# Performance work log

Hardware: AMD Instinct MI355X
Metric: run time of the kernel (lower is better)

## Reference

```python
import jax, jax.numpy as jnp
import numpy as np

EMBED_DIM = 768
N_HEADS = 12
SEQ_LEN = 577
MAX_REL = 2


def _relative_position_indices(seq_len: int, max_rel: int) -> jnp.ndarray:
    """Static [S, S] int index map into the relative bias table."""
    n_patches = seq_len - 1
    n_per_dim = int(np.sqrt(n_patches))
    n_entries = (2 * max_rel - 1) ** 2
    cls_cls, cls_patch, patch_cls = n_entries, n_entries + 1, n_entries + 2
    idx = np.arange(seq_len)
    qy, qx = (idx - 1) // n_per_dim, (idx - 1) % n_per_dim
    ry = np.clip(qy[:, None] - qy[None, :], -max_rel + 1, max_rel - 1)
    rx = np.clip(qx[:, None] - qx[None, :], -max_rel + 1, max_rel - 1)
    patch_idx = (ry + max_rel - 1) * (2 * max_rel - 1) + (rx + max_rel - 1)
    is_cls = idx == 0
    out = np.where(is_cls[None, :], patch_cls, patch_idx)
    out = np.where(is_cls[:, None], cls_patch, out)
    out = np.where(is_cls[:, None] & is_cls[None, :], cls_cls, out)
    return jnp.asarray(out, dtype=jnp.int32)


def setup_inputs() -> dict:
    key = jax.random.key(0)
    ks = jax.random.split(key, 6)
    e = EMBED_DIM
    scale = 1.0 / np.sqrt(e)
    return {
        "x": jax.random.normal(ks[0], (32, SEQ_LEN, e), dtype=jnp.float32),
        "Wq": jax.random.normal(ks[1], (e, e), dtype=jnp.float32) * scale,
        "Wk": jax.random.normal(ks[2], (e, e), dtype=jnp.float32) * scale,
        "Wv": jax.random.normal(ks[3], (e, e), dtype=jnp.float32) * scale,
        "Wo": jax.random.normal(ks[4], (e, e), dtype=jnp.float32) * scale,
        "bo": jnp.zeros((e,), dtype=jnp.float32),
        "bias_table": jax.random.normal(ks[5], (12,), dtype=jnp.float32) * 0.02,
    }


def reference(x, Wq, Wk, Wv, Wo, bo, bias_table):
    b, s, e = x.shape
    h, d = N_HEADS, e // N_HEADS
    rel_idx = _relative_position_indices(s, MAX_REL)  # [S, S] int32 (static)

    q = (x @ Wq).reshape(b, s, h, d).transpose(0, 2, 1, 3)  # [b,h,s,d]
    k = (x @ Wk).reshape(b, s, h, d).transpose(0, 2, 1, 3)
    v = (x @ Wv).reshape(b, s, h, d).transpose(0, 2, 1, 3)

    scores = jnp.einsum('bhqd,bhkd->bhqk', q, k) / jnp.sqrt(jnp.float32(d))
    bias = jnp.take(bias_table, rel_idx, axis=0)  # [S, S]
    attn = jax.nn.softmax(scores + bias[None, None, :, :], axis=-1)

    out = jnp.einsum('bhqk,bhkd->bhqd', attn, v)
    out = out.transpose(0, 2, 1, 3).reshape(b, s, e)
    return out @ Wo + bo
```

## Files before the change

kernel.cpp:

```cpp
#include <hip/hip_runtime.h>

typedef unsigned short u16;
typedef short short8 __attribute__((ext_vector_type(8)));
typedef float floatx4 __attribute__((ext_vector_type(4)));

#define MFMA16(a, b, c) __builtin_amdgcn_mfma_f32_16x16x32_bf16((a), (b), (c), 0, 0, 0)

__device__ __forceinline__ u16 f2bf(float f) {
  unsigned u = __builtin_bit_cast(unsigned, f);
  u = (u + 0x7fffu + ((u >> 16) & 1u)) >> 16;
  return (u16)u;
}

__device__ __forceinline__ float bf2f(u16 u) {
  return __builtin_bit_cast(float, ((unsigned)u) << 16);
}

__device__ __forceinline__ float exp2hw(float x) {
  float r; asm("v_exp_f32 %0, %1" : "=v"(r) : "v"(x)); return r;
}

__device__ __forceinline__ unsigned cvtpk_bf16(float lo, float hi) {
  unsigned r;
  asm("v_cvt_pk_bf16_f32 %0, %1, %2" : "=v"(r) : "v"(lo), "v"(hi));
  return r;
}

__device__ __forceinline__ float bflo(unsigned u) {
  return __builtin_bit_cast(float, u << 16);
}
__device__ __forceinline__ float bfhi(unsigned u) {
  return __builtin_bit_cast(float, u & 0xffff0000u);
}

__device__ __forceinline__ void gload16(const void* g, void* l) {
  typedef __attribute__((address_space(1))) const void GV;
  typedef __attribute__((address_space(3))) void LV;
  __builtin_amdgcn_global_load_lds((GV*)g, (LV*)l, 16, 0, 0);
}


__global__ void cvt_x_kernel(const float* __restrict__ x, u16* __restrict__ xb, int n4) {
  int i = blockIdx.x * 256 + threadIdx.x;
  if (i >= n4) return;
  float4 v = ((const float4*)x)[i];
  ushort4 r; r.x = f2bf(v.x); r.y = f2bf(v.y); r.z = f2bf(v.z); r.w = f2bf(v.w);
  ((ushort4*)xb)[i] = r;
}

__global__ void cvt_wT4_kernel(const float* __restrict__ w0, const float* __restrict__ w1,
                               const float* __restrict__ w2, const float* __restrict__ w3,
                               u16* __restrict__ o0, u16* __restrict__ o3) {
  __shared__ float tile[64][65];
  const int z = blockIdx.z;
  const float* in = (z == 0) ? w0 : (z == 1) ? w1 : (z == 2) ? w2 : w3;
  u16* out = (z == 3) ? o3 : o0 + (size_t)z * 768 * 768;
  const int k0 = blockIdx.x * 64, n0 = blockIdx.y * 64;
  const int t = threadIdx.x;
  const int tr = t >> 6, tc = t & 63;
#pragma unroll
  for (int i = 0; i < 16; ++i) {
    int row = i * 4 + tr;
    tile[row][tc] = in[(size_t)(k0 + row) * 768 + n0 + tc];
  }
  __syncthreads();
#pragma unroll
  for (int i = 0; i < 16; ++i) {
    int row = i * 4 + tr;
    out[(size_t)(n0 + row) * 768 + k0 + tc] = f2bf(tile[tc][row]);
  }
}

__global__ void bias_kernel(const float* __restrict__ table, u16* __restrict__ bp) {
  int idx = blockIdx.x * 256 + threadIdx.x;
  if (idx >= 577 * 76) return;
  int q = idx / 76, kb = idx - q * 76;
  u16 o8[8];
#pragma unroll
  for (int j = 0; j < 8; ++j) {
    int k = kb * 8 + j;
    float v = 0.f;
    if (k <= 576) {
      int id;
      if (q == 0 && k == 0) id = 9;
      else if (q == 0) id = 10;
      else if (k == 0) id = 11;
      else {
        int qy = (q - 1) / 24, qx = (q - 1) % 24;
        int ky = (k - 1) / 24, kx = (k - 1) % 24;
        int ry = qy - ky; ry = ry < -1 ? -1 : (ry > 1 ? 1 : ry);
        int rx = qx - kx; rx = rx < -1 ? -1 : (rx > 1 ? 1 : rx);
        id = (ry + 1) * 3 + (rx + 1);
      }
      v = table[id] * 1.4426950408889634f;
    }
    o8[j] = f2bf(v);
  }
  *(uint4*)(bp + ((size_t)kb * 577 + q) * 8) = *(const uint4*)o8;
}

__global__ void bias576_kernel(const float* __restrict__ table, float* __restrict__ b576) {
  int q = blockIdx.x * 256 + threadIdx.x;
  if (q >= 577) return;
  int id;
  if (q == 0) id = 10;
  else {
    int qy = (q - 1) / 24, qx = (q - 1) % 24;
    int ry = qy - 23; ry = ry < -1 ? -1 : (ry > 1 ? 1 : ry);
    int rx = qx - 23; rx = rx < -1 ? -1 : (rx > 1 ? 1 : rx);
    id = (ry + 1) * 3 + (rx + 1);
  }
  b576[q] = table[id] * 1.4426950408889634f;
}


template <int MODE>
__global__ __launch_bounds__(512, 2) void gemm_kernel(
    const u16* __restrict__ A, const u16* __restrict__ BT,
    const int M, const int NBN,
    float* __restrict__ outF, const float* __restrict__ bvec,
    u16* __restrict__ qarr, u16* __restrict__ karr, u16* __restrict__ vTa) {
  constexpr int K = 768;
  __shared__ __align__(16) u16 smem[33792];
  u16* As = smem;
  u16* Bs = smem + 16384;
  u16* Cs = smem;

  const int nwg = gridDim.x;
  const int q8 = nwg >> 3, r8 = nwg & 7;
  const int xcd = blockIdx.x & 7, jj = blockIdx.x >> 3;
  const int bid = ((xcd < r8) ? xcd * (q8 + 1) : r8 * (q8 + 1) + (xcd - r8) * q8) + jj;

  const int nb = bid % NBN, mb = bid / NBN;
  const int tid = threadIdx.x;
  const int wid = tid >> 6, l = tid & 63;
  const int wrm = wid >> 2, wcn = wid & 3;
  const int l15 = l & 15, l4 = l >> 4;
  const int m0 = mb * 256, n0 = nb * 256;

  floatx4 acc[8][4];
#pragma unroll
  for (int i = 0; i < 8; ++i)
#pragma unroll
    for (int j = 0; j < 4; ++j) acc[i][j] = 0.f;

  const int r1 = tid >> 2;
  const int g1 = (tid & 3) * 8;

  auto stage = [&](int buf, int kt) {
    const int k0 = kt * 32 + g1;
    int ar0 = m0 + r1;       if (ar0 >= M) ar0 = M - 1;
    int ar1 = m0 + r1 + 128; if (ar1 >= M) ar1 = M - 1;
    gload16(A + (size_t)ar0 * K + k0, &As[buf * 8192 + tid * 8]);
    gload16(A + (size_t)ar1 * K + k0, &As[buf * 8192 + 4096 + tid * 8]);
    gload16(BT + (size_t)(n0 + r1) * K + k0, &Bs[buf * 8192 + tid * 8]);
    gload16(BT + (size_t)(n0 + r1 + 128) * K + k0, &Bs[buf * 8192 + 4096 + tid * 8]);
  };

  stage(0, 0);
  __syncthreads();
  int cur = 0;
  for (int kt = 0; kt < 24; ++kt) {
    if (kt + 1 < 24) stage(cur ^ 1, kt + 1);
    short8 af[8], bf[4];
#pragma unroll
    for (int mi = 0; mi < 8; ++mi)
      af[mi] = *(const short8*)&As[cur * 8192 + (wrm * 128 + mi * 16 + l15) * 32 + l4 * 8];
#pragma unroll
    for (int ni = 0; ni < 4; ++ni)
      bf[ni] = *(const short8*)&Bs[cur * 8192 + (wcn * 64 + ni * 16 + l15) * 32 + l4 * 8];
#pragma unroll
    for (int mi = 0; mi < 8; ++mi)
#pragma unroll
      for (int ni = 0; ni < 4; ++ni)
        acc[mi][ni] = MFMA16(af[mi], bf[ni], acc[mi][ni]);
    __syncthreads();
    cur ^= 1;
  }

  if constexpr (MODE == 0) {
    const int proj = nb / 3;
    const int h0 = (nb - proj * 3) * 4;
    const float qs = (proj == 0) ? 0.18033688011112042f : 1.0f;
#pragma unroll
    for (int p = 0; p < 2; ++p) {
      __syncthreads();
      if (wrm == p) {
#pragma unroll
        for (int mi = 0; mi < 8; ++mi)
#pragma unroll
          for (int i = 0; i < 4; ++i) {
            const int rloc = mi * 16 + l4 * 4 + i;
#pragma unroll
            for (int ni = 0; ni < 4; ++ni)
              Cs[rloc * 264 + wcn * 64 + ni * 16 + l15] = f2bf(acc[mi][ni][i] * qs);
          }
      }
      __syncthreads();
      const int r = tid & 127, ch = tid >> 7;
      const int mrow = m0 + p * 128 + r;
      if (mrow < M) {
        const int bq = mrow / 577, sq = mrow - bq * 577;
        const u16* src = Cs + r * 264 + ch * 64;
        if (proj < 2) {
          u16* dst = (proj == 0) ? qarr : karr;
          u16* base = dst + ((size_t)(bq * 12 + h0 + ch) * 577 + sq) * 64;
#pragma unroll
          for (int j2 = 0; j2 < 8; ++j2)
            *(uint4*)(base + j2 * 8) = *(const uint4*)(src + j2 * 8);
        } else {
          u16* vbase = vTa + ((size_t)(bq * 12 + h0 + ch) * 64) * 608 + sq;
#pragma unroll
          for (int dc = 0; dc < 8; ++dc) {
            const short8 vv = *(const short8*)(src + dc * 8);
#pragma unroll
            for (int jx = 0; jx < 8; ++jx)
              vbase[(size_t)(dc * 8 + jx) * 608] = (u16)vv[jx];
          }
        }
      }
    }
  } else {
#pragma unroll
    for (int mi = 0; mi < 8; ++mi) {
#pragma unroll
      for (int i = 0; i < 4; ++i) {
        const int mrow = m0 + wrm * 128 + mi * 16 + l4 * 4 + i;
        if (mrow >= M) continue;
#pragma unroll
        for (int ni = 0; ni < 4; ++ni) {
          const int ncol = n0 + wcn * 64 + ni * 16 + l15;
          outF[(size_t)mrow * 768 + ncol] = acc[mi][ni][i] + bvec[ncol];
        }
      }
    }
  }
}


__global__ __launch_bounds__(256, 3) void attn_kernel(
    const u16* __restrict__ qg, const u16* __restrict__ kg,
    const u16* __restrict__ vT, const u16* __restrict__ bp,
    const float* __restrict__ b576, u16* __restrict__ xa) {
  const int bid = (blockIdx.x & 7) * 240 + (blockIdx.x >> 3);
  const int bh = bid / 5, qblk = bid - bh * 5;
  const int tid = threadIdx.x;
  const int w = tid >> 6, l = tid & 63;
  const int l15 = l & 15, l4 = l >> 4;
  const int qbase = qblk * 128 + w * 32;

  const u16* qh = qg + (size_t)bh * 577 * 64;
  const u16* kh = kg + (size_t)bh * 577 * 64;
  const u16* vh = vT + (size_t)bh * 64 * 608;

  __shared__ u16 Ks[2][64 * 64];
  __shared__ u16 Vs[2][64 * 64];

  const int sr = tid >> 3;
  const int sb = tid & 7;
  const int ss = ((sr & 7) ^ ((2 * (sr >> 3)) & 7)) & 7;
  const int scol = (sb ^ ss) * 8;

  const int sig = ((l15 >> 2) << 3) + (l15 & 3);
  const int s0_ = ((l15 & 3) ^ ((2 * (l15 >> 2)) & 7)) & 7;
  const int s4_ = s0_ ^ 4;
  const int oK00 = sig * 64 + ((l4 ^ s0_) << 3);
  const int oK01 = sig * 64 + (((l4 + 4) ^ s0_) << 3);
  const int oK10 = (sig + 4) * 64 + ((l4 ^ s4_) << 3);
  const int oK11 = (sig + 4) * 64 + (((l4 + 4) ^ s4_) << 3);
  int oV[4][2];
#pragma unroll
  for (int df = 0; df < 4; ++df) {
    const int r = df * 16 + l15;
    const int sv = ((r & 7) ^ ((2 * (r >> 3)) & 7)) & 7;
    oV[df][0] = r * 64 + ((l4 ^ sv) << 3);
    oV[df][1] = r * 64 + (((l4 + 4) ^ sv) << 3);
  }

  short8 qf[2][2];
  int bq[2];
#pragma unroll
  for (int g = 0; g < 2; ++g) {
    int qr = qbase + g * 16 + l15; if (qr > 576) qr = 576;
    bq[g] = qr;
    qf[g][0] = *(const short8*)(qh + qr * 64 + l4 * 8);
    qf[g][1] = *(const short8*)(qh + qr * 64 + 32 + l4 * 8);
  }

  float m[2], lsum[2] = {1.f, 1.f};
  {
    const u16* kp = kh + 576 * 64 + l4 * 8;
    const short8 kA = *(const short8*)(kp);
    const short8 kB = *(const short8*)(kp + 32);
#pragma unroll
    for (int g = 0; g < 2; ++g) {
      float acc = 0.f;
#pragma unroll
      for (int j = 0; j < 8; ++j)
        acc += bf2f((u16)qf[g][0][j]) * bf2f((u16)kA[j]) +
               bf2f((u16)qf[g][1][j]) * bf2f((u16)kB[j]);
      acc += __shfl_xor(acc, 16);
      acc += __shfl_xor(acc, 32);
      m[g] = acc + b576[bq[g]];
    }
  }
  floatx4 o[2][4];
#pragma unroll
  for (int df = 0; df < 4; ++df)
#pragma unroll
    for (int i = 0; i < 4; ++i) {
      const float v5 = bf2f(vh[(size_t)(df * 16 + l4 * 4 + i) * 608 + 576]);
      o[0][df][i] = v5; o[1][df][i] = v5;
    }

  gload16(kh + (size_t)sr * 64 + scol, &Ks[0][sr * 64 + sb * 8]);
  gload16(kh + (size_t)(sr + 32) * 64 + scol, &Ks[0][(sr + 32) * 64 + sb * 8]);
  gload16(vh + (size_t)sr * 608 + scol, &Vs[0][sr * 64 + sb * 8]);
  gload16(vh + (size_t)(sr + 32) * 608 + scol, &Vs[0][(sr + 32) * 64 + sb * 8]);
  __syncthreads();

  for (int t = 0; t < 9; ++t) {
    const int cur = t & 1;
    if (t < 8) {
      const int nk = (t + 1) * 64;
      gload16(kh + (size_t)(nk + sr) * 64 + scol, &Ks[cur ^ 1][sr * 64 + sb * 8]);
      gload16(kh + (size_t)(nk + sr + 32) * 64 + scol, &Ks[cur ^ 1][(sr + 32) * 64 + sb * 8]);
      gload16(vh + (size_t)sr * 608 + nk + scol, &Vs[cur ^ 1][sr * 64 + sb * 8]);
      gload16(vh + (size_t)(sr + 32) * 608 + nk + scol, &Vs[cur ^ 1][(sr + 32) * 64 + sb * 8]);
    }

    const u16* kb_ = &Ks[cur][0];
    const short8 K00 = *(const short8*)(kb_ + oK00);
    const short8 K01 = *(const short8*)(kb_ + oK01);
    const short8 K10 = *(const short8*)(kb_ + oK10);
    const short8 K11 = *(const short8*)(kb_ + oK11);
    const short8 K20 = *(const short8*)(kb_ + oK00 + 32 * 64);
    const short8 K21 = *(const short8*)(kb_ + oK01 + 32 * 64);
    const short8 K30 = *(const short8*)(kb_ + oK10 + 32 * 64);
    const short8 K31 = *(const short8*)(kb_ + oK11 + 32 * 64);

    floatx4 sA0[2], sA1[2], sB0[2], sB1[2];
    __builtin_amdgcn_s_setprio(1);
#pragma unroll
    for (int g = 0; g < 2; ++g) {
      floatx4 a0 = 0.f, a1 = 0.f, b0 = 0.f, b1 = 0.f;
      a0 = MFMA16(K00, qf[g][0], a0); a0 = MFMA16(K01, qf[g][1], a0);
      a1 = MFMA16(K10, qf[g][0], a1); a1 = MFMA16(K11, qf[g][1], a1);
      b0 = MFMA16(K20, qf[g][0], b0); b0 = MFMA16(K21, qf[g][1], b0);
      b1 = MFMA16(K30, qf[g][0], b1); b1 = MFMA16(K31, qf[g][1], b1);
      sA0[g] = a0; sA1[g] = a1; sB0[g] = b0; sB1[g] = b1;
    }
    __builtin_amdgcn_s_setprio(0);

    const int kba = t * 8 + l4;
    const uint4 ba0 = *(const uint4*)(bp + ((size_t)kba * 577 + bq[0]) * 8);
    const uint4 bb0 = *(const uint4*)(bp + ((size_t)(kba + 4) * 577 + bq[0]) * 8);
    const uint4 ba1 = *(const uint4*)(bp + ((size_t)kba * 577 + bq[1]) * 8);
    const uint4 bb1 = *(const uint4*)(bp + ((size_t)(kba + 4) * 577 + bq[1]) * 8);

    float v_[2][16];
#pragma unroll
    for (int g = 0; g < 2; ++g) {
      const uint4 ba = (g == 0) ? ba0 : ba1;
      const uint4 bb = (g == 0) ? bb0 : bb1;
      v_[g][0] = sA0[g][0] + bflo(ba.x);  v_[g][1] = sA0[g][1] + bfhi(ba.x);
      v_[g][2] = sA0[g][2] + bflo(ba.y);  v_[g][3] = sA0[g][3] + bfhi(ba.y);
      v_[g][4] = sA1[g][0] + bflo(ba.z);  v_[g][5] = sA1[g][1] + bfhi(ba.z);
      v_[g][6] = sA1[g][2] + bflo(ba.w);  v_[g][7] = sA1[g][3] + bfhi(ba.w);
      v_[g][8]  = sB0[g][0] + bflo(bb.x); v_[g][9]  = sB0[g][1] + bfhi(bb.x);
      v_[g][10] = sB0[g][2] + bflo(bb.y); v_[g][11] = sB0[g][3] + bfhi(bb.y);
      v_[g][12] = sB1[g][0] + bflo(bb.z); v_[g][13] = sB1[g][1] + bfhi(bb.z);
      v_[g][14] = sB1[g][2] + bflo(bb.w); v_[g][15] = sB1[g][3] + bfhi(bb.w);
    }

    float vm[2];
#pragma unroll
    for (int g = 0; g < 2; ++g) {
      float m0_ = fmaxf(v_[g][0], v_[g][1]),  m1_ = fmaxf(v_[g][2], v_[g][3]);
      float m2_ = fmaxf(v_[g][4], v_[g][5]),  m3_ = fmaxf(v_[g][6], v_[g][7]);
      float m4_ = fmaxf(v_[g][8], v_[g][9]),  m5_ = fmaxf(v_[g][10], v_[g][11]);
      float m6_ = fmaxf(v_[g][12], v_[g][13]), m7_ = fmaxf(v_[g][14], v_[g][15]);
      float a = fmaxf(fmaxf(m0_, m1_), fmaxf(m2_, m3_));
      float b = fmaxf(fmaxf(m4_, m5_), fmaxf(m6_, m7_));
      a = fmaxf(a, b);
      a = fmaxf(a, __shfl_xor(a, 16));
      a = fmaxf(a, __shfl_xor(a, 32));
      vm[g] = a;
    }

    if (__any((vm[0] > m[0] + 8.f) || (vm[1] > m[1] + 8.f))) {
      const float mn0 = fmaxf(m[0], vm[0]), mn1 = fmaxf(m[1], vm[1]);
      const float sc0 = exp2hw(m[0] - mn0), sc1 = exp2hw(m[1] - mn1);
      lsum[0] *= sc0; lsum[1] *= sc1;
#pragma unroll
      for (int df = 0; df < 4; ++df) { o[0][df] *= sc0; o[1][df] *= sc1; }
      m[0] = mn0; m[1] = mn1;
    }

    union PU { unsigned u[4]; short8 s; };
    PU pA[2], pB[2];
#pragma unroll
    for (int g = 0; g < 2; ++g) {
#pragma unroll
      for (int j = 0; j < 16; ++j) v_[g][j] = exp2hw(v_[g][j] - m[g]);
      float s0 = (v_[g][0] + v_[g][1]) + (v_[g][2] + v_[g][3]);
      float s1 = (v_[g][4] + v_[g][5]) + (v_[g][6] + v_[g][7]);
      float s2 = (v_[g][8] + v_[g][9]) + (v_[g][10] + v_[g][11]);
      float s3 = (v_[g][12] + v_[g][13]) + (v_[g][14] + v_[g][15]);
      float rs = (s0 + s1) + (s2 + s3);
      rs += __shfl_xor(rs, 16);
      rs += __shfl_xor(rs, 32);
      lsum[g] += rs;
#pragma unroll
      for (int j = 0; j < 4; ++j) {
        pA[g].u[j] = cvtpk_bf16(v_[g][2 * j], v_[g][2 * j + 1]);
        pB[g].u[j] = cvtpk_bf16(v_[g][8 + 2 * j], v_[g][8 + 2 * j + 1]);
      }
    }

    const u16* vb_ = &Vs[cur][0];
    const short8 vA0 = *(const short8*)(vb_ + oV[0][0]);
    const short8 vB0 = *(const short8*)(vb_ + oV[0][1]);
    const short8 vA1 = *(const short8*)(vb_ + oV[1][0]);
    const short8 vB1 = *(const short8*)(vb_ + oV[1][1]);
    const short8 vA2 = *(const short8*)(vb_ + oV[2][0]);
    const short8 vB2 = *(const short8*)(vb_ + oV[2][1]);
    const short8 vA3 = *(const short8*)(vb_ + oV[3][0]);
    const short8 vB3 = *(const short8*)(vb_ + oV[3][1]);

    __builtin_amdgcn_s_setprio(1);
#pragma unroll
    for (int g = 0; g < 2; ++g) {
      o[g][0] = MFMA16(vA0, pA[g].s, o[g][0]); o[g][0] = MFMA16(vB0, pB[g].s, o[g][0]);
      o[g][1] = MFMA16(vA1, pA[g].s, o[g][1]); o[g][1] = MFMA16(vB1, pB[g].s, o[g][1]);
      o[g][2] = MFMA16(vA2, pA[g].s, o[g][2]); o[g][2] = MFMA16(vB2, pB[g].s, o[g][2]);
      o[g][3] = MFMA16(vA3, pA[g].s, o[g][3]); o[g][3] = MFMA16(vB3, pB[g].s, o[g][3]);
    }
    __builtin_amdgcn_s_setprio(0);

    __syncthreads();
  }

  const int b = bh / 12, h = bh - (bh / 12) * 12;
#pragma unroll
  for (int g = 0; g < 2; ++g) {
    const int gq = qbase + g * 16 + l15;
    if (gq < 577) {
      const float inv = 1.f / lsum[g];
      u16* op = xa + ((size_t)(b * 577 + gq)) * 768 + h * 64 + l4 * 4;
#pragma unroll
      for (int d = 0; d < 4; ++d) {
        unsigned w0 = cvtpk_bf16(o[g][d][0] * inv, o[g][d][1] * inv);
        unsigned w1 = cvtpk_bf16(o[g][d][2] * inv, o[g][d][3] * inv);
        *(unsigned*)(op + d * 16) = w0;
        *(unsigned*)(op + d * 16 + 2) = w1;
      }
    }
  }
}


extern "C" void kernel_launch(void* const* d_in, const int* in_sizes, int n_in,
                              void* d_out, int out_size, void* d_ws, size_t ws_size,
                              hipStream_t stream) {
  const float* x  = (const float*)d_in[0];
  const float* Wq = (const float*)d_in[1];
  const float* Wk = (const float*)d_in[2];
  const float* Wv = (const float*)d_in[3];
  const float* Wo = (const float*)d_in[4];
  const float* bo = (const float*)d_in[5];
  const float* bt = (const float*)d_in[6];
  float* out = (float*)d_out;

  char* ws = (char*)d_ws;
  size_t off = 0;
  auto alloc = [&](size_t bytes) {
    void* p = ws + off;
    off += (bytes + 255) & ~(size_t)255;
    return p;
  };
  u16* xb   = (u16*)alloc((size_t)18464 * 768 * 2);
  u16* WT   = (u16*)alloc((size_t)2304 * 768 * 2);
  u16* WoT  = (u16*)alloc((size_t)768 * 768 * 2);
  u16* qa   = (u16*)alloc((size_t)384 * 577 * 64 * 2);
  u16* ka   = (u16*)alloc((size_t)384 * 577 * 64 * 2);
  u16* vT   = (u16*)alloc((size_t)384 * 64 * 608 * 2);
  u16* biasPk = (u16*)alloc((size_t)76 * 577 * 8 * 2);
  float* b576 = (float*)alloc((size_t)577 * 4);
  (void)ws_size; (void)in_sizes; (void)n_in; (void)out_size;

  cvt_x_kernel<<<(18464 * 768 / 4 + 255) / 256, 256, 0, stream>>>(x, xb, 18464 * 768 / 4);
  dim3 tg4(12, 12, 4);
  cvt_wT4_kernel<<<tg4, 256, 0, stream>>>(Wq, Wk, Wv, Wo, WT, WoT);
  bias_kernel<<<(577 * 76 + 255) / 256, 256, 0, stream>>>(bt, biasPk);
  bias576_kernel<<<3, 256, 0, stream>>>(bt, b576);

  gemm_kernel<0><<<73 * 9, 512, 0, stream>>>(xb, WT, 18464, 9,
                                             nullptr, nullptr, qa, ka, vT);
  attn_kernel<<<1920, 256, 0, stream>>>(qa, ka, vT, biasPk, b576, xb);
  gemm_kernel<1><<<73 * 3, 512, 0, stream>>>(xb, WoT, 18464, 3,
                                             out, bo, nullptr, nullptr, nullptr);
}
```

Measured before the change: 217.5 us.

## Triple-buffer GEMM LDS pipeline with split A/B staging and MFMA priority

Replaces the double-buffered GEMM main loop with a three-slot LDS ring that prefetches two k-tiles ahead. Each iteration is split into two halves, with A staged before the first half and B before the second, and loads are tracked by explicit vmcnt waits and raw barriers. MFMA blocks run under raised wave priority. This needs more LDS (96KB), so launch bounds drop to one 512-thread block per CU, which gives up occupancy in exchange for deeper load/compute overlap.

```diff
diff --git a/kernel.cpp b/kernel.cpp
--- a/kernel.cpp
+++ b/kernel.cpp
@@ -115,15 +115,13 @@
 
 
 template <int MODE>
-__global__ __launch_bounds__(512, 2) void gemm_kernel(
+__global__ __launch_bounds__(512, 1) void gemm_kernel(
     const u16* __restrict__ A, const u16* __restrict__ BT,
     const int M, const int NBN,
     float* __restrict__ outF, const float* __restrict__ bvec,
     u16* __restrict__ qarr, u16* __restrict__ karr, u16* __restrict__ vTa) {
   constexpr int K = 768;
-  __shared__ __align__(16) u16 smem[33792];
-  u16* As = smem;
-  u16* Bs = smem + 16384;
+  __shared__ __align__(16) u16 smem[49152];
   u16* Cs = smem;
 
   const int nwg = gridDim.x;
@@ -146,36 +144,70 @@
 
   const int r1 = tid >> 2;
   const int g1 = (tid & 3) * 8;
-
-  auto stage = [&](int buf, int kt) {
-    const int k0 = kt * 32 + g1;
-    int ar0 = m0 + r1;       if (ar0 >= M) ar0 = M - 1;
-    int ar1 = m0 + r1 + 128; if (ar1 >= M) ar1 = M - 1;
-    gload16(A + (size_t)ar0 * K + k0, &As[buf * 8192 + tid * 8]);
-    gload16(A + (size_t)ar1 * K + k0, &As[buf * 8192 + 4096 + tid * 8]);
-    gload16(BT + (size_t)(n0 + r1) * K + k0, &Bs[buf * 8192 + tid * 8]);
-    gload16(BT + (size_t)(n0 + r1 + 128) * K + k0, &Bs[buf * 8192 + 4096 + tid * 8]);
+  int ar0 = m0 + r1;       if (ar0 >= M) ar0 = M - 1;
+  int ar1 = m0 + r1 + 128; if (ar1 >= M) ar1 = M - 1;
+  const u16* pa0 = A + (size_t)ar0 * K + g1;
+  const u16* pa1 = A + (size_t)ar1 * K + g1;
+  const u16* pb0 = BT + (size_t)(n0 + r1) * K + g1;
+  const u16* pb1 = BT + (size_t)(n0 + r1 + 128) * K + g1;
+
+  auto stageA = [&](int sl, int kt) {
+    const int k0 = kt * 32;
+    gload16(pa0 + k0, &smem[sl * 8192 + tid * 8]);
+    gload16(pa1 + k0, &smem[sl * 8192 + 4096 + tid * 8]);
   };
-
-  stage(0, 0);
-  __syncthreads();
-  int cur = 0;
-  for (int kt = 0; kt < 24; ++kt) {
-    if (kt + 1 < 24) stage(cur ^ 1, kt + 1);
-    short8 af[8], bf[4];
+  auto stageB = [&](int sl, int kt) {
+    const int k0 = kt * 32;
+    gload16(pb0 + k0, &smem[24576 + sl * 8192 + tid * 8]);
+    gload16(pb1 + k0, &smem[24576 + sl * 8192 + 4096 + tid * 8]);
+  };
+
+  stageA(0, 0); stageB(0, 0);
+  stageA(1, 1); stageB(1, 1);
+  asm volatile("s_waitcnt vmcnt(4)" ::: "memory");
+  __builtin_amdgcn_s_barrier();
+
+  int rd = 0, st = 2;
+#pragma unroll 1
+  for (int s = 0; s < 24; ++s) {
+    const u16* sa = &smem[rd * 8192];
+    const u16* sbb = &smem[24576 + rd * 8192];
+
+    if (s < 22) stageA(st, s + 2);
+    short8 af[8], bf01[2];
 #pragma unroll
     for (int mi = 0; mi < 8; ++mi)
-      af[mi] = *(const short8*)&As[cur * 8192 + (wrm * 128 + mi * 16 + l15) * 32 + l4 * 8];
-#pragma unroll
-    for (int ni = 0; ni < 4; ++ni)
-      bf[ni] = *(const short8*)&Bs[cur * 8192 + (wcn * 64 + ni * 16 + l15) * 32 + l4 * 8];
-#pragma unroll
-    for (int mi = 0; mi < 8; ++mi)
-#pragma unroll
-      for (int ni = 0; ni < 4; ++ni)
-        acc[mi][ni] = MFMA16(af[mi], bf[ni], acc[mi][ni]);
-    __syncthreads();
-    cur ^= 1;
+      af[mi] = *(const short8*)&sa[(wrm * 128 + mi * 16 + l15) * 32 + l4 * 8];
+#pragma unroll
+    for (int ni = 0; ni < 2; ++ni)
+      bf01[ni] = *(const short8*)&sbb[(wcn * 64 + ni * 16 + l15) * 32 + l4 * 8];
+    __builtin_amdgcn_s_setprio(1);
+#pragma unroll
+    for (int mi = 0; mi < 8; ++mi) {
+      acc[mi][0] = MFMA16(af[mi], bf01[0], acc[mi][0]);
+      acc[mi][1] = MFMA16(af[mi], bf01[1], acc[mi][1]);
+    }
+    __builtin_amdgcn_s_setprio(0);
+    __builtin_amdgcn_s_barrier();
+
+    if (s < 22) stageB(st, s + 2);
+    short8 bf23[2];
+#pragma unroll
+    for (int ni = 0; ni < 2; ++ni)
+      bf23[ni] = *(const short8*)&sbb[(wcn * 64 + (ni + 2) * 16 + l15) * 32 + l4 * 8];
+    __builtin_amdgcn_s_setprio(1);
+#pragma unroll
+    for (int mi = 0; mi < 8; ++mi) {
+      acc[mi][2] = MFMA16(af[mi], bf23[0], acc[mi][2]);
+      acc[mi][3] = MFMA16(af[mi], bf23[1], acc[mi][3]);
+    }
+    __builtin_amdgcn_s_setprio(0);
+    if (s < 22)       asm volatile("s_waitcnt vmcnt(4)" ::: "memory");
+    else if (s == 22) asm volatile("s_waitcnt vmcnt(0)" ::: "memory");
+    __builtin_amdgcn_s_barrier();
+
+    rd = (rd == 2) ? 0 : rd + 1;
+    st = (st == 2) ? 0 : st + 1;
   }
 
   if constexpr (MODE == 0) {
```

After: 225.9 us. 3.9% more time.
